# Kernel optimization log

Hardware: AMD Instinct MI355X
Metric: run time of the kernel (lower is better)

## Reference

```python
import jax, jax.numpy as jnp
import numpy as np

EMBED = 1024
HEADS = 16
HDIM = 64
FFN = 4 * EMBED
EPS = 1e-5


def setup_inputs() -> dict:
    key = jax.random.key(0)
    ks = jax.random.split(key, 12)
    def lin(k, fan_in, shape):
        b = 1.0 / np.sqrt(fan_in)
        return jax.random.uniform(k, shape, jnp.float32, -b, b)
    return {
        "x": jax.random.normal(ks[0], (4, 2048, EMBED), jnp.float32),
        "Wq": lin(ks[1], EMBED, (EMBED, HEADS * HDIM)),
        "Wk": lin(ks[2], EMBED, (EMBED, HEADS * HDIM)),
        "Wv": lin(ks[3], EMBED, (EMBED, HEADS * HDIM)),
        "Wo": lin(ks[4], HEADS * HDIM, (HEADS * HDIM, EMBED)),
        "ln1_g": jnp.ones((EMBED,), jnp.float32),
        "ln1_b": jnp.zeros((EMBED,), jnp.float32),
        "ln2_g": jnp.ones((EMBED,), jnp.float32),
        "ln2_b": jnp.zeros((EMBED,), jnp.float32),
        "W1": lin(ks[5], EMBED, (EMBED, FFN)),
        "b1": lin(ks[6], EMBED, (FFN,)),
        "W2": lin(ks[7], FFN, (FFN, EMBED)),
        "b2": lin(ks[8], FFN, (EMBED,)),
    }


def _layer_norm(x, g, b):
    mu = jnp.mean(x, axis=-1, keepdims=True)
    var = jnp.var(x, axis=-1, keepdims=True)
    return (x - mu) * jax.lax.rsqrt(var + EPS) * g + b


def reference(x, Wq, Wk, Wv, Wo, ln1_g, ln1_b, ln2_g, ln2_b, W1, b1, W2, b2):
    B, S, _ = x.shape
    residual = x
    h = _layer_norm(x, ln1_g, ln1_b)
    # project and split heads: [B, H, S, Dh]
    q = (h @ Wq).reshape(B, S, HEADS, HDIM).transpose(0, 2, 1, 3)
    k = (h @ Wk).reshape(B, S, HEADS, HDIM).transpose(0, 2, 1, 3)
    v = (h @ Wv).reshape(B, S, HEADS, HDIM).transpose(0, 2, 1, 3)
    scale = HDIM ** -0.5
    scores = jnp.einsum("bhqd,bhkd->bhqk", q, k) * scale
    # causal mask (upper triangle excluded above diagonal -> -inf)
    mask = jnp.triu(jnp.ones((S, S), bool), k=1)
    scores = jnp.where(mask, -jnp.inf, scores)
    attn = jax.nn.softmax(scores, axis=-1)
    out = jnp.einsum("bhqk,bhkd->bhqd", attn, v)
    out = out.transpose(0, 2, 1, 3).reshape(B, S, HEADS * HDIM)
    x = residual + out @ Wo
    residual = x
    h = _layer_norm(x, ln2_g, ln2_b)
    h = jax.nn.gelu(h @ W1 + b1, approximate=False) @ W2 + b2
    return residual + h
```

## Files before the change

### kernel.cpp

```cpp
#include <hip/hip_runtime.h>
#include <hip/hip_bf16.h>
#include <math.h>

typedef __bf16 bf16;
typedef bf16 bf16x8 __attribute__((ext_vector_type(8)));
typedef bf16 bf16x4 __attribute__((ext_vector_type(4)));
typedef float f32x4 __attribute__((ext_vector_type(4)));

#define ROWS 8192
#define EMB  1024
#define NH   16
#define HD   64
#define FFN  4096
#define QKVN 3072
#define SEQ  2048

__device__ __forceinline__ void gl2lds16(const bf16* g, bf16* l) {
  __builtin_amdgcn_global_load_lds((const __attribute__((address_space(1))) void*)g,
                                   (__attribute__((address_space(3))) void*)l, 16, 0, 0);
}

__global__ void transpose_cast(const float* __restrict__ W, bf16* __restrict__ Wt,
                               int K, int N, float scale) {
  __shared__ float tile[32][33];
  const int n0 = blockIdx.x * 32, k0 = blockIdx.y * 32;
  const int tx = threadIdx.x & 31, ty = threadIdx.x >> 5;
#pragma unroll
  for (int i = 0; i < 32; i += 8)
    tile[ty + i][tx] = W[(size_t)(k0 + ty + i) * N + n0 + tx];
  __syncthreads();
#pragma unroll
  for (int i = 0; i < 32; i += 8)
    Wt[(size_t)(n0 + ty + i) * K + k0 + tx] = (bf16)(tile[tx][ty + i] * scale);
}

__global__ void transpose_cast4(const float* __restrict__ W0, const float* __restrict__ W1,
                                const float* __restrict__ W2, const float* __restrict__ W3,
                                bf16* __restrict__ dst) {
  __shared__ float tile[32][33];
  const int z = blockIdx.z;
  const float* W = (z == 0) ? W0 : (z == 1) ? W1 : (z == 2) ? W2 : W3;
  const float scale = (z == 0) ? 0.125f : 1.0f;
  bf16* Wt = dst + (size_t)z * EMB * EMB;
  const int n0 = blockIdx.x * 32, k0 = blockIdx.y * 32;
  const int tx = threadIdx.x & 31, ty = threadIdx.x >> 5;
#pragma unroll
  for (int i = 0; i < 32; i += 8)
    tile[ty + i][tx] = W[(size_t)(k0 + ty + i) * EMB + n0 + tx];
  __syncthreads();
#pragma unroll
  for (int i = 0; i < 32; i += 8)
    Wt[(size_t)(n0 + ty + i) * EMB + k0 + tx] = (bf16)(tile[tx][ty + i] * scale);
}

__global__ __launch_bounds__(256) void layernorm_bf16(
    const float* __restrict__ x, const float* __restrict__ g,
    const float* __restrict__ b, bf16* __restrict__ out) {
  const int row = blockIdx.x * 4 + (threadIdx.x >> 6);
  const int lane = threadIdx.x & 63;
  const float4* xr = (const float4*)(x + (size_t)row * EMB);
  float4 v[4];
  float s = 0.f, ss = 0.f;
#pragma unroll
  for (int k = 0; k < 4; k++) {
    v[k] = xr[lane + 64 * k];
    s += v[k].x + v[k].y + v[k].z + v[k].w;
    ss += v[k].x * v[k].x + v[k].y * v[k].y + v[k].z * v[k].z + v[k].w * v[k].w;
  }
#pragma unroll
  for (int off = 32; off; off >>= 1) {
    s += __shfl_xor(s, off);
    ss += __shfl_xor(ss, off);
  }
  const float mu = s * (1.0f / EMB);
  const float rs = rsqrtf(ss * (1.0f / EMB) - mu * mu + 1e-5f);
  bf16* orow = out + (size_t)row * EMB;
#pragma unroll
  for (int k = 0; k < 4; k++) {
    const float4 gv = ((const float4*)g)[lane + 64 * k];
    const float4 bv = ((const float4*)b)[lane + 64 * k];
    bf16x4 o;
    o[0] = (bf16)((v[k].x - mu) * rs * gv.x + bv.x);
    o[1] = (bf16)((v[k].y - mu) * rs * gv.y + bv.y);
    o[2] = (bf16)((v[k].z - mu) * rs * gv.z + bv.z);
    o[3] = (bf16)((v[k].w - mu) * rs * gv.w + bv.w);
    *(bf16x4*)(orow + (size_t)(lane + 64 * k) * 4) = o;
  }
}

template <int EPI, int N_, int K_>
__global__ __launch_bounds__(256, 2) void gemm_bt(
    const bf16* __restrict__ A, const bf16* __restrict__ Bt, void* __restrict__ C,
    const float* __restrict__ bias, const float* __restrict__ resid,
    bf16* __restrict__ vt) {
  constexpr int N = N_, K = K_;
  __shared__ __align__(16) bf16 As[128 * 64];
  __shared__ __align__(16) bf16 Bs[128 * 64];
  const int tid = threadIdx.x;
  const int lane = tid & 63;
  const int wave = tid >> 6;
  const int wm = (wave >> 1) * 64;
  const int wn = (wave & 1) * 64;
  constexpr int tn = N / 128;
  const int lin = blockIdx.y * tn + blockIdx.x;
  const int xcd = lin & 7;
  const int idx = lin >> 3;
  const int m0 = (xcd * 8 + (idx & 7)) * 128;
  const int n0 = (idx >> 3) * 128;
  const int quad = lane >> 4;
  const int l16 = lane & 15;
  const int srow8 = lane >> 3;
  const int scol = ((lane & 7) ^ srow8) * 8;
  const int xr = l16 & 7;

  const bf16* ap = A + (size_t)(m0 + wave * 32 + srow8) * K + scol;
  const bf16* bp = Bt + (size_t)(n0 + wave * 32 + srow8) * K + scol;
  bf16* const as0 = &As[wave * 32 * 64];
  bf16* const bs0 = &Bs[wave * 32 * 64];

  f32x4 acc[4][4] = {};

  for (int kt = 0; kt < K; kt += 64) {
    __syncthreads();
#pragma unroll
    for (int q = 0; q < 4; q++) {
      gl2lds16(ap + q * 8 * K, as0 + q * 8 * 64);
      gl2lds16(bp + q * 8 * K, bs0 + q * 8 * 64);
    }
    ap += 64;
    bp += 64;
    __syncthreads();
#pragma unroll
    for (int h = 0; h < 2; h++) {
      const int cp = ((h * 4 + quad) ^ xr) * 8;
      bf16x8 af[4], bfr[4];
#pragma unroll
      for (int i = 0; i < 4; i++)
        af[i] = *(const bf16x8*)&As[(wm + i * 16 + l16) * 64 + cp];
#pragma unroll
      for (int j = 0; j < 4; j++)
        bfr[j] = *(const bf16x8*)&Bs[(wn + j * 16 + l16) * 64 + cp];
#pragma unroll
      for (int i = 0; i < 4; i++)
#pragma unroll
        for (int j = 0; j < 4; j++)
          acc[i][j] = __builtin_amdgcn_mfma_f32_16x16x32_bf16(af[i], bfr[j], acc[i][j], 0, 0, 0);
    }
  }

  if (EPI == 4 && n0 >= 2 * EMB) {
#pragma unroll
    for (int i = 0; i < 4; i++)
#pragma unroll
      for (int j = 0; j < 4; j++) {
        const int col = n0 + wn + j * 16 + l16;
        const int c2 = col - 2 * EMB;
        const int h_ = c2 >> 6, d = c2 & 63;
        const int row0 = m0 + wm + i * 16 + quad * 4;
        const int b_ = row0 >> 11, s = row0 & (SEQ - 1);
        bf16x4 o;
        o[0] = (bf16)acc[i][j][0];
        o[1] = (bf16)acc[i][j][1];
        o[2] = (bf16)acc[i][j][2];
        o[3] = (bf16)acc[i][j][3];
        *(bf16x4*)(vt + ((size_t)((b_ * 16 + h_) * 64 + d)) * SEQ + s) = o;
      }
    return;
  }

#pragma unroll
  for (int i = 0; i < 4; i++)
#pragma unroll
    for (int j = 0; j < 4; j++)
#pragma unroll
      for (int r = 0; r < 4; r++) {
        const int row = m0 + wm + i * 16 + quad * 4 + r;
        const int col = n0 + wn + j * 16 + l16;
        const size_t idx2 = (size_t)row * N + col;
        float v = acc[i][j][r];
        if (EPI == 0 || EPI == 4) {
          ((bf16*)C)[idx2] = (bf16)v;
        } else if (EPI == 1) {
          ((float*)C)[idx2] = v + resid[idx2];
        } else if (EPI == 2) {
          v += bias[col];
          const float u = 1.5957691216f * (v + 0.044715f * v * v * v);
          v = v / (1.0f + __expf(-u));
          ((bf16*)C)[idx2] = (bf16)v;
        } else {
          ((float*)C)[idx2] = v + bias[col] + resid[idx2];
        }
      }
}

__global__ __launch_bounds__(256, 6) void flash_attn(
    const bf16* __restrict__ qkv, const bf16* __restrict__ vt, bf16* __restrict__ out) {
  const int bid = blockIdx.x;
  const int xcd = bid & 7;
  const int idx = bid >> 3;
  const int pr = idx & 15;
  const int bh = xcd + ((idx >> 4) << 3);
  const int b = bh >> 4, h = bh & 15;
  const int tid = threadIdx.x;
  const int lane = tid & 63, wave = tid >> 6;
  const int quad = lane >> 4, l16 = lane & 15;

  __shared__ __align__(16) bf16 Ks[64 * 64];
  __shared__ __align__(16) bf16 Vts[64 * 64];
  __shared__ __align__(16) bf16 Ps[4][16][72];

  const size_t rowbase = (size_t)b * SEQ;
  const int s8 = (lane >> 3) & 7;
  const int cs = ((lane & 7) ^ s8) * 8;
  const int xk = l16 & 7;
  const bf16* kbase = qkv + rowbase * QKVN + EMB + h * HD;
  const bf16* vbase = vt + (size_t)(bh * HD) * SEQ;

#pragma unroll 1
  for (int half = 0; half < 2; half++) {
    const int qt = half ? pr : 31 - pr;
    const int qrow_a = qt * 64 + wave * 16 + l16;
    const bf16* qptr = qkv + (rowbase + qrow_a) * QKVN + h * HD;
    const bf16x8 qf0 = *(const bf16x8*)(qptr + quad * 8);
    const bf16x8 qf1 = *(const bf16x8*)(qptr + 32 + quad * 8);
    f32x4 o0 = {}, o1 = {}, o2 = {}, o3 = {};
    f32x4 lsum = {};
    const int qrow_c = qt * 64 + wave * 16 + quad * 4;

    const bf16* kp = kbase + (size_t)(wave * 8 + s8) * QKVN + cs;
    const bf16* vp = vbase + (size_t)(wave * 8 + s8) * SEQ + cs;

#pragma unroll 1
    for (int kt = 0; kt <= qt; kt++) {
      __syncthreads();
      gl2lds16(kp + (size_t)kt * 64 * QKVN, &Ks[(wave * 8) * 64]);
      gl2lds16(kp + (size_t)(kt * 64 + 32) * QKVN, &Ks[(32 + wave * 8) * 64]);
      gl2lds16(vp + kt * 64, &Vts[(wave * 8) * 64]);
      gl2lds16(vp + (size_t)32 * SEQ + kt * 64, &Vts[(32 + wave * 8) * 64]);
      __syncthreads();

      if (kt < qt) {
#pragma unroll
        for (int j = 0; j < 4; j++) {
          const int rr = (j * 16 + l16) * 64;
          const bf16x8 kf0 = *(const bf16x8*)&Ks[rr + (quad ^ xk) * 8];
          const bf16x8 kf1 = *(const bf16x8*)&Ks[rr + ((4 + quad) ^ xk) * 8];
          f32x4 a = {};
          a = __builtin_amdgcn_mfma_f32_16x16x32_bf16(qf0, kf0, a, 0, 0, 0);
          a = __builtin_amdgcn_mfma_f32_16x16x32_bf16(qf1, kf1, a, 0, 0, 0);
#pragma unroll
          for (int r = 0; r < 4; r++) {
            const float pj = __expf(a[r]);
            lsum[r] += pj;
            Ps[wave][quad * 4 + r][j * 16 + l16] = (bf16)pj;
          }
        }
      } else {
#pragma unroll
        for (int j = 0; j < 4; j++) {
          if (j > wave) {
#pragma unroll
            for (int r = 0; r < 4; r++)
              Ps[wave][quad * 4 + r][j * 16 + l16] = (bf16)0.0f;
          } else {
            const int rr = (j * 16 + l16) * 64;
            const bf16x8 kf0 = *(const bf16x8*)&Ks[rr + (quad ^ xk) * 8];
            const bf16x8 kf1 = *(const bf16x8*)&Ks[rr + ((4 + quad) ^ xk) * 8];
            f32x4 a = {};
            a = __builtin_amdgcn_mfma_f32_16x16x32_bf16(qf0, kf0, a, 0, 0, 0);
            a = __builtin_amdgcn_mfma_f32_16x16x32_bf16(qf1, kf1, a, 0, 0, 0);
            if (j == wave) {
#pragma unroll
              for (int r = 0; r < 4; r++) {
                const float v = (l16 > quad * 4 + r) ? -INFINITY : a[r];
                const float pj = __expf(v);
                lsum[r] += pj;
                Ps[wave][quad * 4 + r][j * 16 + l16] = (bf16)pj;
              }
            } else {
#pragma unroll
              for (int r = 0; r < 4; r++) {
                const float pj = __expf(a[r]);
                lsum[r] += pj;
                Ps[wave][quad * 4 + r][j * 16 + l16] = (bf16)pj;
              }
            }
          }
        }
      }

      const bf16x8 af0 = *(const bf16x8*)&Ps[wave][l16][quad * 8];
      const bf16x8 af1 = *(const bf16x8*)&Ps[wave][l16][32 + quad * 8];
#pragma unroll
      for (int j = 0; j < 4; j++) {
        const int rr = (j * 16 + l16) * 64;
        const bf16x8 vf0 = *(const bf16x8*)&Vts[rr + (quad ^ xk) * 8];
        const bf16x8 vf1 = *(const bf16x8*)&Vts[rr + ((4 + quad) ^ xk) * 8];
        f32x4& oj = (j == 0) ? o0 : (j == 1) ? o1 : (j == 2) ? o2 : o3;
        oj = __builtin_amdgcn_mfma_f32_16x16x32_bf16(af0, vf0, oj, 0, 0, 0);
        oj = __builtin_amdgcn_mfma_f32_16x16x32_bf16(af1, vf1, oj, 0, 0, 0);
      }
    }

#pragma unroll
    for (int r = 0; r < 4; r++) {
      float ls = lsum[r];
      ls += __shfl_xor(ls, 1);
      ls += __shfl_xor(ls, 2);
      ls += __shfl_xor(ls, 4);
      ls += __shfl_xor(ls, 8);
      const float iv = 1.0f / ls;
      bf16* op = out + (rowbase + qrow_c + r) * EMB + h * HD;
      op[0 + l16] = (bf16)(o0[r] * iv);
      op[16 + l16] = (bf16)(o1[r] * iv);
      op[32 + l16] = (bf16)(o2[r] * iv);
      op[48 + l16] = (bf16)(o3[r] * iv);
    }
  }
}

extern "C" void kernel_launch(void* const* d_in, const int* in_sizes, int n_in,
                              void* d_out, int out_size, void* d_ws, size_t ws_size,
                              hipStream_t stream) {
  const float* x     = (const float*)d_in[0];
  const float* Wq    = (const float*)d_in[1];
  const float* Wk    = (const float*)d_in[2];
  const float* Wv    = (const float*)d_in[3];
  const float* Wo    = (const float*)d_in[4];
  const float* ln1_g = (const float*)d_in[5];
  const float* ln1_b = (const float*)d_in[6];
  const float* ln2_g = (const float*)d_in[7];
  const float* ln2_b = (const float*)d_in[8];
  const float* W1    = (const float*)d_in[9];
  const float* b1    = (const float*)d_in[10];
  const float* W2    = (const float*)d_in[11];
  const float* b2    = (const float*)d_in[12];
  float* out = (float*)d_out;

  bf16* p = (bf16*)d_ws;
  bf16* wqkv_t = p;                 p += (size_t)QKVN * EMB;
  bf16* wo_t   = p;                 p += (size_t)EMB * EMB;
  bf16* w1_t   = p;                 p += (size_t)FFN * EMB;
  bf16* w2_t   = p;                 p += (size_t)EMB * FFN;
  bf16* h      = p;                 p += (size_t)ROWS * EMB;
  bf16* qkv    = p;                 p += (size_t)ROWS * QKVN;
  bf16* attn_o = p;                 p += (size_t)ROWS * EMB;
  bf16* ffn1   = p;
  bf16* vt     = w1_t;

  transpose_cast4<<<dim3(32, 32, 4), 256, 0, stream>>>(Wq, Wk, Wv, Wo, wqkv_t);

  layernorm_bf16<<<ROWS / 4, 256, 0, stream>>>(x, ln1_g, ln1_b, h);

  gemm_bt<4, QKVN, EMB><<<dim3(QKVN / 128, ROWS / 128), 256, 0, stream>>>(
      h, wqkv_t, qkv, nullptr, nullptr, vt);

  flash_attn<<<1024, 256, 0, stream>>>(qkv, vt, attn_o);

  transpose_cast<<<dim3(128, 32), 256, 0, stream>>>(W1, w1_t, EMB, FFN, 1.0f);
  transpose_cast<<<dim3(32, 128), 256, 0, stream>>>(W2, w2_t, FFN, EMB, 1.0f);

  gemm_bt<1, EMB, EMB><<<dim3(EMB / 128, ROWS / 128), 256, 0, stream>>>(
      attn_o, wo_t, out, nullptr, x, nullptr);

  layernorm_bf16<<<ROWS / 4, 256, 0, stream>>>(out, ln2_g, ln2_b, h);

  gemm_bt<2, FFN, EMB><<<dim3(FFN / 128, ROWS / 128), 256, 0, stream>>>(
      h, w1_t, ffn1, b1, nullptr, nullptr);

  gemm_bt<3, EMB, FFN><<<dim3(EMB / 128, ROWS / 128), 256, 0, stream>>>(
      ffn1, w2_t, out, b2, out, nullptr);
}
```

Before: 465.2 us.

## Split flash attention to one query tile per block and separate V transpose

Flash attention now launches 2048 blocks, each handling a single query tile, where before each block processed a paired long and short tile. The V transpose is taken out of the QKV GEMM epilogue and done in its own tiled transpose kernel, writing into the free LN buffer. The W1/W2 casts are moved ahead because vt no longer aliases w1_t. This adds a kernel launch and an extra pass over V, and it gives up the paired tile load balancing in exchange for more parallelism and a simpler GEMM epilogue.

```diff
diff --git a/kernel.cpp b/kernel.cpp
--- a/kernel.cpp
+++ b/kernel.cpp
@@ -53,6 +53,20 @@
     Wt[(size_t)(n0 + ty + i) * EMB + k0 + tx] = (bf16)(tile[tx][ty + i] * scale);
 }
 
+__global__ void v_transpose(const bf16* __restrict__ qkv, bf16* __restrict__ vt) {
+  __shared__ bf16 tile[32][33];
+  const int s0 = blockIdx.x * 32, d0 = blockIdx.y * 32, bh = blockIdx.z;
+  const int b = bh >> 4, h = bh & 15;
+  const int tx = threadIdx.x & 31, ty = threadIdx.x >> 5;
+#pragma unroll
+  for (int i = 0; i < 32; i += 8)
+    tile[ty + i][tx] = qkv[(size_t)(b * SEQ + s0 + ty + i) * QKVN + 2 * EMB + h * HD + d0 + tx];
+  __syncthreads();
+#pragma unroll
+  for (int i = 0; i < 32; i += 8)
+    vt[(size_t)(bh * HD + d0 + ty + i) * SEQ + s0 + tx] = tile[tx][ty + i];
+}
+
 __global__ __launch_bounds__(256) void layernorm_bf16(
     const float* __restrict__ x, const float* __restrict__ g,
     const float* __restrict__ b, bf16* __restrict__ out) {
@@ -91,8 +105,7 @@
 template <int EPI, int N_, int K_>
 __global__ __launch_bounds__(256, 2) void gemm_bt(
     const bf16* __restrict__ A, const bf16* __restrict__ Bt, void* __restrict__ C,
-    const float* __restrict__ bias, const float* __restrict__ resid,
-    bf16* __restrict__ vt) {
+    const float* __restrict__ bias, const float* __restrict__ resid) {
   constexpr int N = N_, K = K_;
   __shared__ __align__(16) bf16 As[128 * 64];
   __shared__ __align__(16) bf16 Bs[128 * 64];
@@ -148,26 +161,6 @@
     }
   }
 
-  if (EPI == 4 && n0 >= 2 * EMB) {
-#pragma unroll
-    for (int i = 0; i < 4; i++)
-#pragma unroll
-      for (int j = 0; j < 4; j++) {
-        const int col = n0 + wn + j * 16 + l16;
-        const int c2 = col - 2 * EMB;
-        const int h_ = c2 >> 6, d = c2 & 63;
-        const int row0 = m0 + wm + i * 16 + quad * 4;
-        const int b_ = row0 >> 11, s = row0 & (SEQ - 1);
-        bf16x4 o;
-        o[0] = (bf16)acc[i][j][0];
-        o[1] = (bf16)acc[i][j][1];
-        o[2] = (bf16)acc[i][j][2];
-        o[3] = (bf16)acc[i][j][3];
-        *(bf16x4*)(vt + ((size_t)((b_ * 16 + h_) * 64 + d)) * SEQ + s) = o;
-      }
-    return;
-  }
-
 #pragma unroll
   for (int i = 0; i < 4; i++)
 #pragma unroll
@@ -178,7 +171,7 @@
         const int col = n0 + wn + j * 16 + l16;
         const size_t idx2 = (size_t)row * N + col;
         float v = acc[i][j][r];
-        if (EPI == 0 || EPI == 4) {
+        if (EPI == 0) {
           ((bf16*)C)[idx2] = (bf16)v;
         } else if (EPI == 1) {
           ((float*)C)[idx2] = v + resid[idx2];
@@ -198,8 +191,8 @@
   const int bid = blockIdx.x;
   const int xcd = bid & 7;
   const int idx = bid >> 3;
-  const int pr = idx & 15;
-  const int bh = xcd + ((idx >> 4) << 3);
+  const int qt = 31 - (idx & 31);
+  const int bh = xcd + ((idx >> 5) << 3);
   const int b = bh >> 4, h = bh & 15;
   const int tid = threadIdx.x;
   const int lane = tid & 63, wave = tid >> 6;
@@ -216,106 +209,102 @@
   const bf16* kbase = qkv + rowbase * QKVN + EMB + h * HD;
   const bf16* vbase = vt + (size_t)(bh * HD) * SEQ;
 
+  const int qrow_a = qt * 64 + wave * 16 + l16;
+  const bf16* qptr = qkv + (rowbase + qrow_a) * QKVN + h * HD;
+  const bf16x8 qf0 = *(const bf16x8*)(qptr + quad * 8);
+  const bf16x8 qf1 = *(const bf16x8*)(qptr + 32 + quad * 8);
+  f32x4 o0 = {}, o1 = {}, o2 = {}, o3 = {};
+  f32x4 lsum = {};
+  const int qrow_c = qt * 64 + wave * 16 + quad * 4;
+
+  const bf16* kp = kbase + (size_t)(wave * 8 + s8) * QKVN + cs;
+  const bf16* vp = vbase + (size_t)(wave * 8 + s8) * SEQ + cs;
+
 #pragma unroll 1
-  for (int half = 0; half < 2; half++) {
-    const int qt = half ? pr : 31 - pr;
-    const int qrow_a = qt * 64 + wave * 16 + l16;
-    const bf16* qptr = qkv + (rowbase + qrow_a) * QKVN + h * HD;
-    const bf16x8 qf0 = *(const bf16x8*)(qptr + quad * 8);
-    const bf16x8 qf1 = *(const bf16x8*)(qptr + 32 + quad * 8);
-    f32x4 o0 = {}, o1 = {}, o2 = {}, o3 = {};
-    f32x4 lsum = {};
-    const int qrow_c = qt * 64 + wave * 16 + quad * 4;
-
-    const bf16* kp = kbase + (size_t)(wave * 8 + s8) * QKVN + cs;
-    const bf16* vp = vbase + (size_t)(wave * 8 + s8) * SEQ + cs;
-
-#pragma unroll 1
-    for (int kt = 0; kt <= qt; kt++) {
-      __syncthreads();
-      gl2lds16(kp + (size_t)kt * 64 * QKVN, &Ks[(wave * 8) * 64]);
-      gl2lds16(kp + (size_t)(kt * 64 + 32) * QKVN, &Ks[(32 + wave * 8) * 64]);
-      gl2lds16(vp + kt * 64, &Vts[(wave * 8) * 64]);
-      gl2lds16(vp + (size_t)32 * SEQ + kt * 64, &Vts[(32 + wave * 8) * 64]);
-      __syncthreads();
-
-      if (kt < qt) {
-#pragma unroll
-        for (int j = 0; j < 4; j++) {
+  for (int kt = 0; kt <= qt; kt++) {
+    __syncthreads();
+    gl2lds16(kp + (size_t)kt * 64 * QKVN, &Ks[(wave * 8) * 64]);
+    gl2lds16(kp + (size_t)(kt * 64 + 32) * QKVN, &Ks[(32 + wave * 8) * 64]);
+    gl2lds16(vp + kt * 64, &Vts[(wave * 8) * 64]);
+    gl2lds16(vp + (size_t)32 * SEQ + kt * 64, &Vts[(32 + wave * 8) * 64]);
+    __syncthreads();
+
+    if (kt < qt) {
+#pragma unroll
+      for (int j = 0; j < 4; j++) {
+        const int rr = (j * 16 + l16) * 64;
+        const bf16x8 kf0 = *(const bf16x8*)&Ks[rr + (quad ^ xk) * 8];
+        const bf16x8 kf1 = *(const bf16x8*)&Ks[rr + ((4 + quad) ^ xk) * 8];
+        f32x4 a = {};
+        a = __builtin_amdgcn_mfma_f32_16x16x32_bf16(qf0, kf0, a, 0, 0, 0);
+        a = __builtin_amdgcn_mfma_f32_16x16x32_bf16(qf1, kf1, a, 0, 0, 0);
+#pragma unroll
+        for (int r = 0; r < 4; r++) {
+          const float pj = __expf(a[r]);
+          lsum[r] += pj;
+          Ps[wave][quad * 4 + r][j * 16 + l16] = (bf16)pj;
+        }
+      }
+    } else {
+#pragma unroll
+      for (int j = 0; j < 4; j++) {
+        if (j > wave) {
+#pragma unroll
+          for (int r = 0; r < 4; r++)
+            Ps[wave][quad * 4 + r][j * 16 + l16] = (bf16)0.0f;
+        } else {
           const int rr = (j * 16 + l16) * 64;
           const bf16x8 kf0 = *(const bf16x8*)&Ks[rr + (quad ^ xk) * 8];
           const bf16x8 kf1 = *(const bf16x8*)&Ks[rr + ((4 + quad) ^ xk) * 8];
           f32x4 a = {};
           a = __builtin_amdgcn_mfma_f32_16x16x32_bf16(qf0, kf0, a, 0, 0, 0);
           a = __builtin_amdgcn_mfma_f32_16x16x32_bf16(qf1, kf1, a, 0, 0, 0);
-#pragma unroll
-          for (int r = 0; r < 4; r++) {
-            const float pj = __expf(a[r]);
-            lsum[r] += pj;
-            Ps[wave][quad * 4 + r][j * 16 + l16] = (bf16)pj;
-          }
-        }
-      } else {
-#pragma unroll
-        for (int j = 0; j < 4; j++) {
-          if (j > wave) {
-#pragma unroll
-            for (int r = 0; r < 4; r++)
-              Ps[wave][quad * 4 + r][j * 16 + l16] = (bf16)0.0f;
+          if (j == wave) {
+#pragma unroll
+            for (int r = 0; r < 4; r++) {
+              const float v = (l16 > quad * 4 + r) ? -INFINITY : a[r];
+              const float pj = __expf(v);
+              lsum[r] += pj;
+              Ps[wave][quad * 4 + r][j * 16 + l16] = (bf16)pj;
+            }
           } else {
-            const int rr = (j * 16 + l16) * 64;
-            const bf16x8 kf0 = *(const bf16x8*)&Ks[rr + (quad ^ xk) * 8];
-            const bf16x8 kf1 = *(const bf16x8*)&Ks[rr + ((4 + quad) ^ xk) * 8];
-            f32x4 a = {};
-            a = __builtin_amdgcn_mfma_f32_16x16x32_bf16(qf0, kf0, a, 0, 0, 0);
-            a = __builtin_amdgcn_mfma_f32_16x16x32_bf16(qf1, kf1, a, 0, 0, 0);
-            if (j == wave) {
-#pragma unroll
-              for (int r = 0; r < 4; r++) {
-                const float v = (l16 > quad * 4 + r) ? -INFINITY : a[r];
-                const float pj = __expf(v);
-                lsum[r] += pj;
-                Ps[wave][quad * 4 + r][j * 16 + l16] = (bf16)pj;
-              }
-            } else {
-#pragma unroll
-              for (int r = 0; r < 4; r++) {
-                const float pj = __expf(a[r]);
-                lsum[r] += pj;
-                Ps[wave][quad * 4 + r][j * 16 + l16] = (bf16)pj;
-              }
+#pragma unroll
+            for (int r = 0; r < 4; r++) {
+              const float pj = __expf(a[r]);
+              lsum[r] += pj;
+              Ps[wave][quad * 4 + r][j * 16 + l16] = (bf16)pj;
             }
           }
         }
       }
-
-      const bf16x8 af0 = *(const bf16x8*)&Ps[wave][l16][quad * 8];
-      const bf16x8 af1 = *(const bf16x8*)&Ps[wave][l16][32 + quad * 8];
-#pragma unroll
-      for (int j = 0; j < 4; j++) {
-        const int rr = (j * 16 + l16) * 64;
-        const bf16x8 vf0 = *(const bf16x8*)&Vts[rr + (quad ^ xk) * 8];
-        const bf16x8 vf1 = *(const bf16x8*)&Vts[rr + ((4 + quad) ^ xk) * 8];
-        f32x4& oj = (j == 0) ? o0 : (j == 1) ? o1 : (j == 2) ? o2 : o3;
-        oj = __builtin_amdgcn_mfma_f32_16x16x32_bf16(af0, vf0, oj, 0, 0, 0);
-        oj = __builtin_amdgcn_mfma_f32_16x16x32_bf16(af1, vf1, oj, 0, 0, 0);
-      }
     }
 
-#pragma unroll
-    for (int r = 0; r < 4; r++) {
-      float ls = lsum[r];
-      ls += __shfl_xor(ls, 1);
-      ls += __shfl_xor(ls, 2);
-      ls += __shfl_xor(ls, 4);
-      ls += __shfl_xor(ls, 8);
-      const float iv = 1.0f / ls;
-      bf16* op = out + (rowbase + qrow_c + r) * EMB + h * HD;
-      op[0 + l16] = (bf16)(o0[r] * iv);
-      op[16 + l16] = (bf16)(o1[r] * iv);
-      op[32 + l16] = (bf16)(o2[r] * iv);
-      op[48 + l16] = (bf16)(o3[r] * iv);
+    const bf16x8 af0 = *(const bf16x8*)&Ps[wave][l16][quad * 8];
+    const bf16x8 af1 = *(const bf16x8*)&Ps[wave][l16][32 + quad * 8];
+#pragma unroll
+    for (int j = 0; j < 4; j++) {
+      const int rr = (j * 16 + l16) * 64;
+      const bf16x8 vf0 = *(const bf16x8*)&Vts[rr + (quad ^ xk) * 8];
+      const bf16x8 vf1 = *(const bf16x8*)&Vts[rr + ((4 + quad) ^ xk) * 8];
+      f32x4& oj = (j == 0) ? o0 : (j == 1) ? o1 : (j == 2) ? o2 : o3;
+      oj = __builtin_amdgcn_mfma_f32_16x16x32_bf16(af0, vf0, oj, 0, 0, 0);
+      oj = __builtin_amdgcn_mfma_f32_16x16x32_bf16(af1, vf1, oj, 0, 0, 0);
     }
+  }
+
+#pragma unroll
+  for (int r = 0; r < 4; r++) {
+    float ls = lsum[r];
+    ls += __shfl_xor(ls, 1);
+    ls += __shfl_xor(ls, 2);
+    ls += __shfl_xor(ls, 4);
+    ls += __shfl_xor(ls, 8);
+    const float iv = 1.0f / ls;
+    bf16* op = out + (rowbase + qrow_c + r) * EMB + h * HD;
+    op[0 + l16] = (bf16)(o0[r] * iv);
+    op[16 + l16] = (bf16)(o1[r] * iv);
+    op[32 + l16] = (bf16)(o2[r] * iv);
+    op[48 + l16] = (bf16)(o3[r] * iv);
   }
 }
 
@@ -346,28 +335,29 @@
   bf16* qkv    = p;                 p += (size_t)ROWS * QKVN;
   bf16* attn_o = p;                 p += (size_t)ROWS * EMB;
   bf16* ffn1   = p;
-  bf16* vt     = w1_t;
+  bf16* vt     = h;
 
   transpose_cast4<<<dim3(32, 32, 4), 256, 0, stream>>>(Wq, Wk, Wv, Wo, wqkv_t);
-
-  layernorm_bf16<<<ROWS / 4, 256, 0, stream>>>(x, ln1_g, ln1_b, h);
-
-  gemm_bt<4, QKVN, EMB><<<dim3(QKVN / 128, ROWS / 128), 256, 0, stream>>>(
-      h, wqkv_t, qkv, nullptr, nullptr, vt);
-
-  flash_attn<<<1024, 256, 0, stream>>>(qkv, vt, attn_o);
-
   transpose_cast<<<dim3(128, 32), 256, 0, stream>>>(W1, w1_t, EMB, FFN, 1.0f);
   transpose_cast<<<dim3(32, 128), 256, 0, stream>>>(W2, w2_t, FFN, EMB, 1.0f);
 
+  layernorm_bf16<<<ROWS / 4, 256, 0, stream>>>(x, ln1_g, ln1_b, h);
+
+  gemm_bt<0, QKVN, EMB><<<dim3(QKVN / 128, ROWS / 128), 256, 0, stream>>>(
+      h, wqkv_t, qkv, nullptr, nullptr);
+
+  v_transpose<<<dim3(SEQ / 32, HD / 32, 64), 256, 0, stream>>>(qkv, vt);
+
+  flash_attn<<<2048, 256, 0, stream>>>(qkv, vt, attn_o);
+
   gemm_bt<1, EMB, EMB><<<dim3(EMB / 128, ROWS / 128), 256, 0, stream>>>(
-      attn_o, wo_t, out, nullptr, x, nullptr);
+      attn_o, wo_t, out, nullptr, x);
 
   layernorm_bf16<<<ROWS / 4, 256, 0, stream>>>(out, ln2_g, ln2_b, h);
 
   gemm_bt<2, FFN, EMB><<<dim3(FFN / 128, ROWS / 128), 256, 0, stream>>>(
-      h, w1_t, ffn1, b1, nullptr, nullptr);
+      h, w1_t, ffn1, b1, nullptr);
 
   gemm_bt<3, EMB, FFN><<<dim3(EMB / 128, ROWS / 128), 256, 0, stream>>>(
-      ffn1, w2_t, out, b2, out, nullptr);
-}
+      ffn1, w2_t, out, b2, out);
+}
```

After: 481.0 us. 1.03x slower.
